# Kernel optimization log

Measured on AMD Instinct MI355X. Metric: run time of the kernel, lower is better.

Reference implementation:

```python
import jax, jax.numpy as jnp
import numpy as np
import math

B, N, E, H = 2, 2048, 1024, 16
K = E // H  # head dim = 64


def setup_inputs() -> dict:
    key = jax.random.key(0)
    ks = jax.random.split(key, 9)
    s = 0.02
    return {
        "x": jax.random.normal(ks[0], (B, N, E), jnp.float32),
        "Wq": jax.random.normal(ks[1], (E, E), jnp.float32) * s,
        "bq": jax.random.normal(ks[2], (E,), jnp.float32) * s,
        "Wk": jax.random.normal(ks[3], (E, E), jnp.float32) * s,
        "bk": jax.random.normal(ks[4], (E,), jnp.float32) * s,
        "Wv": jax.random.normal(ks[5], (E, E), jnp.float32) * s,
        "bv": jax.random.normal(ks[6], (E,), jnp.float32) * s,
        "Wp": jax.random.normal(ks[7], (E, E), jnp.float32) * s,
        "bp": jax.random.normal(ks[8], (E,), jnp.float32) * s,
    }


def _split_heads(t):
    # torch: t.transpose(-1,-2).view(b, H, K, N)  -> (B, H, K, N)
    return t.transpose(0, 2, 1).reshape(t.shape[0], H, K, t.shape[1])


def reference(x, Wq, bq, Wk, bk, Wv, bv, Wp, bp):
    b, n, _ = x.shape
    q = _split_heads(x @ Wq.T + bq)  # (B,H,K,N)
    k = _split_heads(x @ Wk.T + bk)
    v = _split_heads(x @ Wv.T + bv)
    # NOTE: module divides by sqrt(query.size(1)) == sqrt(num_heads), not sqrt(head_dim)
    ctx = jnp.einsum('bhkn,bhkm->bhmn', q, k) / math.sqrt(H)  # (B,H,m=key,n=query)
    mask = jnp.triu(jnp.ones((n, n), dtype=bool), 1)  # True where n(query) > m(key)
    ctx = jnp.where(mask[None, None], -jnp.inf, ctx)
    # faithful to source: softmax over last axis (the query axis n)
    ctx = jax.nn.softmax(ctx, axis=-1)
    out = jnp.einsum('bhmn,bhvm->bhvn', ctx, v)  # (B,H,K,N)
    out = out.reshape(b, E, n).transpose(0, 2, 1)  # (B,N,E)
    return out @ Wp.T + bp
```

## Files before the change

kernel.cpp:

```cpp
#include <hip/hip_runtime.h>
#include <hip/hip_bf16.h>

typedef __hip_bfloat16 bf16;
typedef __attribute__((ext_vector_type(8))) short bf16x8;
typedef __attribute__((ext_vector_type(4))) float f32x4;
typedef __attribute__((ext_vector_type(4))) short s16x4;

constexpr int B_ = 2, N_ = 2048, E_ = 1024, H_ = 16, KD_ = 64;
constexpr int M_ = B_ * N_;
constexpr float SCALE = 0.25f * 1.44269504088896f;

#define MFMA16(A, Bf, C) __builtin_amdgcn_mfma_f32_16x16x32_bf16(A, Bf, C, 0, 0, 0)
#define SBAR() do { __builtin_amdgcn_s_barrier(); __builtin_amdgcn_sched_barrier(0); } while (0)
#define WAITCNT(s) asm volatile("s_waitcnt " s ::: "memory")
#define SETPRIO(p) __builtin_amdgcn_s_setprio(p)

typedef const __attribute__((address_space(1))) void* gptr_t;
typedef __attribute__((address_space(3))) void* sptr_t;

__device__ inline short bf16bits(float f) {
  bf16 h = __float2bfloat16(f);
  short s;
  __builtin_memcpy(&s, &h, 2);
  return s;
}
__device__ inline float bf16f(short s) {
  bf16 h;
  __builtin_memcpy(&h, &s, 2);
  return __bfloat162float(h);
}

template <int NROWS, int NTHR>
__device__ inline void stageT(const bf16* __restrict__ base, int stride_elems,
                              char* lds) {
  const int t = threadIdx.x;
#pragma unroll
  for (int i = 0; i < NROWS * 128 / (NTHR * 16); i++) {
    int L = i * NTHR * 16 + t * 16;
    int row = L >> 7;
    int slot = ((L >> 4) & 7) ^ (row & 7);
    const bf16* src = base + (size_t)row * stride_elems + slot * 8;
    __builtin_amdgcn_global_load_lds((gptr_t)(const void*)src,
                                     (sptr_t)(void*)(lds + L), 16, 0, 0);
  }
}

__device__ inline bf16x8 frag_ld(const char* lds, int row, int ks) {
  const int g = (threadIdx.x >> 4) & 3;
  const int off = (ks * 64 + g * 16) ^ ((row & 7) << 4);
  return *(const bf16x8*)(lds + row * 128 + off);
}

__global__ __launch_bounds__(256) void cvt_all(
    const float* __restrict__ x, const float* __restrict__ wq,
    const float* __restrict__ wk, const float* __restrict__ wv,
    const float* __restrict__ wp, bf16* __restrict__ dst) {
  const size_t XN = (size_t)M_ * E_;
  const size_t WN = (size_t)E_ * E_;
  size_t i = ((size_t)blockIdx.x * 256 + threadIdx.x) * 4;
  const float* src;
  size_t off;
  if (i < XN) { src = x; off = i; }
  else if (i < XN + WN) { src = wq; off = i - XN; }
  else if (i < XN + 2 * WN) { src = wk; off = i - XN - WN; }
  else if (i < XN + 3 * WN) { src = wv; off = i - XN - 2 * WN; }
  else { src = wp; off = i - XN - 3 * WN; }
  float4 v = *(const float4*)(src + off);
  s16x4 o;
  o[0] = bf16bits(v.x); o[1] = bf16bits(v.y);
  o[2] = bf16bits(v.z); o[3] = bf16bits(v.w);
  *(s16x4*)(dst + i) = o;
}

__global__ __launch_bounds__(256) void gemm_qkv(
    const bf16* __restrict__ A, const bf16* __restrict__ Wb,
    const float* __restrict__ bq, const float* __restrict__ bk,
    const float* __restrict__ bv, bf16* __restrict__ Qhd,
    bf16* __restrict__ Khd, bf16* __restrict__ Vtd) {
  __shared__ char Asm[16384];
  __shared__ char Bsm[16384];
  const int t = threadIdx.x, lane = t & 63, w = t >> 6;
  const int wr = w >> 1, wc = w & 1;
  const int c = lane & 15, g = lane >> 4;
  const int row0 = blockIdx.y * 128, col0 = blockIdx.x * 128;
  f32x4 acc[4][4] = {};

  for (int k0 = 0; k0 < E_; k0 += 64) {
    stageT<64, 256>(A + (size_t)row0 * E_ + k0, E_, Asm);
    stageT<64, 256>(A + (size_t)(row0 + 64) * E_ + k0, E_, Asm + 8192);
    stageT<64, 256>(Wb + (size_t)col0 * E_ + k0, E_, Bsm);
    stageT<64, 256>(Wb + (size_t)(col0 + 64) * E_ + k0, E_, Bsm + 8192);
    __syncthreads();
#pragma unroll
    for (int ks = 0; ks < 2; ks++) {
      bf16x8 af[4], bfr[4];
#pragma unroll
      for (int mi = 0; mi < 4; mi++) af[mi] = frag_ld(Asm, wr * 64 + mi * 16 + c, ks);
#pragma unroll
      for (int ni = 0; ni < 4; ni++) bfr[ni] = frag_ld(Bsm, wc * 64 + ni * 16 + c, ks);
#pragma unroll
      for (int mi = 0; mi < 4; mi++)
#pragma unroll
        for (int ni = 0; ni < 4; ni++)
          acc[mi][ni] = MFMA16(af[mi], bfr[ni], acc[mi][ni]);
    }
    __syncthreads();
  }

  const int sel = col0 >> 10;
  const float* biasp = sel == 0 ? bq : sel == 1 ? bk : bv;
  bf16* outp = sel == 0 ? Qhd : sel == 1 ? Khd : Vtd;
#pragma unroll
  for (int mi = 0; mi < 4; mi++) {
#pragma unroll
    for (int ni = 0; ni < 4; ni++) {
      const int row = row0 + wr * 64 + mi * 16 + g * 4;
      const int col = col0 + wc * 64 + ni * 16 + c;
      const int ccol = col & 1023, h = ccol >> 6, kd = ccol & 63;
      const float bvf = biasp[ccol];
      if (sel < 2) {
        const float scl = (sel == 1) ? SCALE : 1.0f;
#pragma unroll
        for (int r = 0; r < 4; r++) {
          const int rr = row + r, b = rr >> 11, n = rr & (N_ - 1);
          outp[(((size_t)(b * H_ + h)) * N_ + n) * KD_ + kd] =
              __float2bfloat16((acc[mi][ni][r] + bvf) * scl);
        }
      } else {
        const int b = row >> 11, n = row & (N_ - 1);
        s16x4 o;
#pragma unroll
        for (int r = 0; r < 4; r++) o[r] = bf16bits(acc[mi][ni][r] + bvf);
        *(s16x4*)&outp[(((size_t)(b * H_ + h)) * KD_ + kd) * N_ + n] = o;
      }
    }
  }
}

__global__ __launch_bounds__(256) void gemm_proj(
    const bf16* __restrict__ A, const bf16* __restrict__ Wb,
    const float* __restrict__ bias, float* __restrict__ outf) {
  __shared__ char Asm[16384];
  __shared__ char Bsm[8192];
  const int t = threadIdx.x, lane = t & 63, w = t >> 6;
  const int wr = w >> 1, wc = w & 1;
  const int c = lane & 15, g = lane >> 4;
  const int row0 = blockIdx.y * 128, col0 = blockIdx.x * 64;
  f32x4 acc[4][2] = {};

  for (int k0 = 0; k0 < E_; k0 += 64) {
    stageT<64, 256>(A + (size_t)row0 * E_ + k0, E_, Asm);
    stageT<64, 256>(A + (size_t)(row0 + 64) * E_ + k0, E_, Asm + 8192);
    stageT<64, 256>(Wb + (size_t)col0 * E_ + k0, E_, Bsm);
    __syncthreads();
#pragma unroll
    for (int ks = 0; ks < 2; ks++) {
      bf16x8 af[4], bfr[2];
#pragma unroll
      for (int mi = 0; mi < 4; mi++) af[mi] = frag_ld(Asm, wr * 64 + mi * 16 + c, ks);
#pragma unroll
      for (int ni = 0; ni < 2; ni++) bfr[ni] = frag_ld(Bsm, wc * 32 + ni * 16 + c, ks);
#pragma unroll
      for (int mi = 0; mi < 4; mi++)
#pragma unroll
        for (int ni = 0; ni < 2; ni++)
          acc[mi][ni] = MFMA16(af[mi], bfr[ni], acc[mi][ni]);
    }
    __syncthreads();
  }

#pragma unroll
  for (int mi = 0; mi < 4; mi++) {
#pragma unroll
    for (int ni = 0; ni < 2; ni++) {
      const int row = row0 + wr * 64 + mi * 16 + g * 4;
      const int col = col0 + wc * 32 + ni * 16 + c;
      const float bvf = bias[col];
#pragma unroll
      for (int r = 0; r < 4; r++)
        outf[(size_t)(row + r) * E_ + col] = acc[mi][ni][r] + bvf;
    }
  }
}

__global__ __launch_bounds__(512, 4) void phaseA(
    const bf16* __restrict__ Kh, const bf16* __restrict__ Qh,
    bf16* __restrict__ Vt) {
  __shared__ char Ksm[8192];
  __shared__ char Qsm[2][16384];
  __shared__ float rbuf[2][64];
  const int t = threadIdx.x, lane = t & 63, w = t >> 6;
  const int c = lane & 15, g = (lane >> 4);
  const int wm = w & 3, wn = w >> 2;
  const int bid = blockIdx.y * 16 + blockIdx.x;
  const int ww = (bid & 7) * 64 + (bid >> 3);
  const int bx = ww & 15, bh = ww >> 4;
  const bf16* Kb = Kh + (size_t)bh * N_ * KD_;
  const bf16* Qb = Qh + (size_t)bh * N_ * KD_;
  bf16* Vtb = Vt + (size_t)bh * KD_ * N_;

#pragma unroll 1
  for (int seg = 0; seg < 2; seg++) {
    const int mb = seg ? (31 - bx) : bx;
    const int m0 = mb * 64;
    const int ntE = mb >> 1;

    WAITCNT("lgkmcnt(0)");
    SBAR();
    stageT<64, 512>(Kb + (size_t)m0 * KD_, KD_, Ksm);
    stageT<128, 512>(Qb, KD_, Qsm[0]);
    WAITCNT("vmcnt(2)");
    SBAR();
    bf16x8 af0 = frag_ld(Ksm, wm * 16 + c, 0);
    bf16x8 af1 = frag_ld(Ksm, wm * 16 + c, 1);
    float sm[4] = {};

#pragma unroll 1
    for (int nt = 0; nt <= ntE; nt++) {
      WAITCNT("vmcnt(0) lgkmcnt(0)");
      SBAR();
      if (nt + 1 <= ntE)
        stageT<128, 512>(Qb + (size_t)(nt + 1) * 128 * KD_, KD_,
                         Qsm[(nt + 1) & 1]);
      const char* qs = Qsm[nt & 1];
      if (nt < ntE) {
#pragma unroll
        for (int nf = 0; nf < 4; nf++) {
          const int ni = wn * 4 + nf;
          bf16x8 b0 = frag_ld(qs, ni * 16 + c, 0);
          bf16x8 b1 = frag_ld(qs, ni * 16 + c, 1);
          SETPRIO(1);
          f32x4 sv = {0.f, 0.f, 0.f, 0.f};
          sv = MFMA16(af0, b0, sv);
          sv = MFMA16(af1, b1, sv);
          SETPRIO(0);
#pragma unroll
          for (int r = 0; r < 4; r++) sm[r] += exp2f(sv[r]);
        }
      } else {
        const int mg = m0 + wm * 16 + g * 4;
#pragma unroll
        for (int nf = 0; nf < 4; nf++) {
          const int ni = wn * 4 + nf;
          bf16x8 b0 = frag_ld(qs, ni * 16 + c, 0);
          bf16x8 b1 = frag_ld(qs, ni * 16 + c, 1);
          SETPRIO(1);
          f32x4 sv = {0.f, 0.f, 0.f, 0.f};
          sv = MFMA16(af0, b0, sv);
          sv = MFMA16(af1, b1, sv);
          SETPRIO(0);
          const int ng = nt * 128 + ni * 16 + c;
#pragma unroll
          for (int r = 0; r < 4; r++) {
            float e = exp2f(sv[r]);
            sm[r] += (ng <= mg + r) ? e : 0.f;
          }
        }
      }
    }

#pragma unroll
    for (int r = 0; r < 4; r++) {
      float v = sm[r];
#pragma unroll
      for (int d = 1; d < 16; d <<= 1) v += __shfl_xor(v, d, 64);
      if (c == 0) rbuf[wn][wm * 16 + g * 4 + r] = v;
    }
    WAITCNT("lgkmcnt(0)");
    SBAR();
    {
      const int kd = t >> 3, mc = (t & 7) * 8;
      bf16* p = Vtb + (size_t)kd * N_ + m0 + mc;
      bf16x8 v = *(const bf16x8*)p;
      bf16x8 o;
#pragma unroll
      for (int j = 0; j < 8; j++) {
        const float inv = 1.0f / (rbuf[0][mc + j] + rbuf[1][mc + j]);
        o[j] = bf16bits(bf16f(v[j]) * inv);
      }
      *(bf16x8*)p = o;
    }
  }
}

__global__ __launch_bounds__(512, 4) void phaseB(
    const bf16* __restrict__ Qh, const bf16* __restrict__ Kh,
    const bf16* __restrict__ Vt, bf16* __restrict__ attn) {
  __shared__ char Ksm[2][8192];
  __shared__ char Vsm[2][8192];
  __shared__ char Psm[8192];
  const int t = threadIdx.x, lane = t & 63, w = t >> 6;
  const int c = lane & 15, g = lane >> 4;
  const int wm = w & 3, wn = w >> 2;
  const int bid = blockIdx.y * 16 + blockIdx.x;
  const int ww = (bid & 7) * 64 + (bid >> 3);
  const int bx = ww & 15, bh = ww >> 4;
  const int b = bh >> 4, h = bh & 15;
  const int NT = N_ / 64;
  const bf16* Qb = Qh + (size_t)bh * N_ * KD_;
  const bf16* Kb = Kh + (size_t)bh * N_ * KD_;
  const bf16* Vb = Vt + (size_t)bh * KD_ * N_;

#pragma unroll 1
  for (int seg = 0; seg < 2; seg++) {
    const int qt = seg ? (31 - bx) : bx;
    const int n0 = qt * 64, mt0 = qt;

    WAITCNT("lgkmcnt(0)");
    SBAR();
    stageT<64, 512>(Qb + (size_t)n0 * KD_, KD_, Psm);
    stageT<64, 512>(Kb + (size_t)mt0 * 64 * KD_, KD_, Ksm[mt0 & 1]);
    stageT<64, 512>(Vb + mt0 * 64, N_, Vsm[mt0 & 1]);
    WAITCNT("vmcnt(2)");
    SBAR();
    bf16x8 qf[2][2];
#pragma unroll
    for (int ni = 0; ni < 2; ni++) {
      qf[ni][0] = frag_ld(Psm, wn * 32 + ni * 16 + c, 0);
      qf[ni][1] = frag_ld(Psm, wn * 32 + ni * 16 + c, 1);
    }
    f32x4 out[2] = {};

    auto do_tile = [&](int mt, bool diag) {
      WAITCNT("vmcnt(0) lgkmcnt(0)");
      SBAR();
      if (mt + 1 < NT) {
        stageT<64, 512>(Kb + (size_t)(mt + 1) * 64 * KD_, KD_, Ksm[(mt + 1) & 1]);
        stageT<64, 512>(Vb + (mt + 1) * 64, N_, Vsm[(mt + 1) & 1]);
      }
      const char* ksm = Ksm[mt & 1];
      bf16x8 kf0 = frag_ld(ksm, wm * 16 + c, 0);
      bf16x8 kf1 = frag_ld(ksm, wm * 16 + c, 1);
      SETPRIO(1);
      f32x4 sv[2];
#pragma unroll
      for (int ni = 0; ni < 2; ni++) {
        f32x4 z = {0.f, 0.f, 0.f, 0.f};
        z = MFMA16(kf0, qf[ni][0], z);
        z = MFMA16(kf1, qf[ni][1], z);
        sv[ni] = z;
      }
      SETPRIO(0);
      const int ml = wm * 16 + g * 4;
#pragma unroll
      for (int ni = 0; ni < 2; ni++) {
        const int nl = wn * 32 + ni * 16 + c;
        s16x4 p;
#pragma unroll
        for (int r = 0; r < 4; r++) {
          float val = exp2f(sv[ni][r]);
          if (diag && nl > (ml + r)) val = 0.f;
          p[r] = bf16bits(val);
        }
        const int off = nl * 128 + ((wm * 32 + g * 8) ^ ((nl & 7) << 4));
        *(s16x4*)(Psm + off) = p;
      }
      WAITCNT("lgkmcnt(0)");
      SBAR();
      const char* vsm = Vsm[mt & 1];
      bf16x8 pa0 = frag_ld(Psm, wm * 16 + c, 0);
      bf16x8 pa1 = frag_ld(Psm, wm * 16 + c, 1);
      SETPRIO(1);
#pragma unroll
      for (int ni = 0; ni < 2; ni++) {
        const int kdrow = wn * 32 + ni * 16 + c;
        bf16x8 v0 = frag_ld(vsm, kdrow, 0);
        bf16x8 v1 = frag_ld(vsm, kdrow, 1);
        out[ni] = MFMA16(pa0, v0, out[ni]);
        out[ni] = MFMA16(pa1, v1, out[ni]);
      }
      SETPRIO(0);
    };

    do_tile(mt0, true);
#pragma unroll 1
    for (int mt = mt0 + 1; mt < NT; mt++) do_tile(mt, false);

#pragma unroll
    for (int ni = 0; ni < 2; ni++) {
#pragma unroll
      for (int r = 0; r < 4; r++) {
        const int n = n0 + wm * 16 + g * 4 + r;
        const int kd = wn * 32 + ni * 16 + c;
        attn[((size_t)(b * N_ + n)) * E_ + h * 64 + kd] =
            __float2bfloat16(out[ni][r]);
      }
    }
  }
}

extern "C" void kernel_launch(void* const* d_in, const int* in_sizes, int n_in,
                              void* d_out, int out_size, void* d_ws, size_t ws_size,
                              hipStream_t stream) {
  (void)in_sizes; (void)n_in; (void)out_size; (void)ws_size;
  const float* x  = (const float*)d_in[0];
  const float* Wq = (const float*)d_in[1];
  const float* bq = (const float*)d_in[2];
  const float* Wk = (const float*)d_in[3];
  const float* bk = (const float*)d_in[4];
  const float* Wv = (const float*)d_in[5];
  const float* bv = (const float*)d_in[6];
  const float* Wp = (const float*)d_in[7];
  const float* bp = (const float*)d_in[8];
  float* out = (float*)d_out;

  const size_t XN = (size_t)M_ * E_;
  const size_t WN = (size_t)E_ * E_;
  const size_t HN = (size_t)B_ * H_ * N_ * KD_;

  bf16* xb   = (bf16*)d_ws;
  bf16* wqkv = xb + XN;
  bf16* wpb  = wqkv + 3 * WN;
  bf16* Qhd  = wpb + WN;
  bf16* Khd  = Qhd + HN;
  bf16* Vtd  = Khd + HN;
  bf16* attn = xb;

  cvt_all<<<dim3(8192), 256, 0, stream>>>(x, Wq, Wk, Wv, Wp, xb);

  gemm_qkv<<<dim3(24, 32), 256, 0, stream>>>(xb, wqkv, bq, bk, bv,
                                             Qhd, Khd, Vtd);

  phaseA<<<dim3(16, B_ * H_), 512, 0, stream>>>(Khd, Qhd, Vtd);
  phaseB<<<dim3(16, B_ * H_), 512, 0, stream>>>(Qhd, Khd, Vtd, attn);

  gemm_proj<<<dim3(16, 32), 256, 0, stream>>>(attn, wpb, bp, out);
}
```

Before: 124.8 us.

## Software-pipeline attention loop: overlap PV of previous tile with QK of current

Splits the per-tile attention body into separate QK and PV stages and interleaves them, so the PV MFMAs for tile mt-1 run alongside the QK and exp work for tile mt. P is double-buffered and V is triple-buffered in shared memory so the prefetched tiles do not overwrite data still being read. This removes one barrier per tile. In exchange, LDS use per block rises from 40 KB to 56 KB, which likely lowers how many blocks fit per CU. The K/V visibility now depends on per-thread vmcnt waits with no barrier before the QK read, which may be a race.

```diff
diff --git a/kernel.cpp b/kernel.cpp
--- a/kernel.cpp
+++ b/kernel.cpp
@@ -287,8 +287,8 @@
     const bf16* __restrict__ Qh, const bf16* __restrict__ Kh,
     const bf16* __restrict__ Vt, bf16* __restrict__ attn) {
   __shared__ char Ksm[2][8192];
-  __shared__ char Vsm[2][8192];
-  __shared__ char Psm[8192];
+  __shared__ char Vsm[3][8192];
+  __shared__ char Psm[2][8192];
   const int t = threadIdx.x, lane = t & 63, w = t >> 6;
   const int c = lane & 15, g = lane >> 4;
   const int wm = w & 3, wn = w >> 2;
@@ -308,26 +308,22 @@
 
     WAITCNT("lgkmcnt(0)");
     SBAR();
-    stageT<64, 512>(Qb + (size_t)n0 * KD_, KD_, Psm);
+    stageT<64, 512>(Qb + (size_t)n0 * KD_, KD_, Psm[0]);
     stageT<64, 512>(Kb + (size_t)mt0 * 64 * KD_, KD_, Ksm[mt0 & 1]);
-    stageT<64, 512>(Vb + mt0 * 64, N_, Vsm[mt0 & 1]);
+    stageT<64, 512>(Vb + mt0 * 64, N_, Vsm[mt0 % 3]);
     WAITCNT("vmcnt(2)");
     SBAR();
     bf16x8 qf[2][2];
 #pragma unroll
     for (int ni = 0; ni < 2; ni++) {
-      qf[ni][0] = frag_ld(Psm, wn * 32 + ni * 16 + c, 0);
-      qf[ni][1] = frag_ld(Psm, wn * 32 + ni * 16 + c, 1);
-    }
+      qf[ni][0] = frag_ld(Psm[0], wn * 32 + ni * 16 + c, 0);
+      qf[ni][1] = frag_ld(Psm[0], wn * 32 + ni * 16 + c, 1);
+    }
+    WAITCNT("lgkmcnt(0)");
+    SBAR();
     f32x4 out[2] = {};
 
-    auto do_tile = [&](int mt, bool diag) {
-      WAITCNT("vmcnt(0) lgkmcnt(0)");
-      SBAR();
-      if (mt + 1 < NT) {
-        stageT<64, 512>(Kb + (size_t)(mt + 1) * 64 * KD_, KD_, Ksm[(mt + 1) & 1]);
-        stageT<64, 512>(Vb + (mt + 1) * 64, N_, Vsm[(mt + 1) & 1]);
-      }
+    auto qk_tile = [&](int mt, bool diag) {
       const char* ksm = Ksm[mt & 1];
       bf16x8 kf0 = frag_ld(ksm, wm * 16 + c, 0);
       bf16x8 kf1 = frag_ld(ksm, wm * 16 + c, 1);
@@ -342,6 +338,7 @@
       }
       SETPRIO(0);
       const int ml = wm * 16 + g * 4;
+      char* ps = Psm[mt & 1];
 #pragma unroll
       for (int ni = 0; ni < 2; ni++) {
         const int nl = wn * 32 + ni * 16 + c;
@@ -353,13 +350,15 @@
           p[r] = bf16bits(val);
         }
         const int off = nl * 128 + ((wm * 32 + g * 8) ^ ((nl & 7) << 4));
-        *(s16x4*)(Psm + off) = p;
-      }
-      WAITCNT("lgkmcnt(0)");
-      SBAR();
-      const char* vsm = Vsm[mt & 1];
-      bf16x8 pa0 = frag_ld(Psm, wm * 16 + c, 0);
-      bf16x8 pa1 = frag_ld(Psm, wm * 16 + c, 1);
+        *(s16x4*)(ps + off) = p;
+      }
+    };
+
+    auto pv_tile = [&](int mt) {
+      const char* ps = Psm[mt & 1];
+      const char* vsm = Vsm[mt % 3];
+      bf16x8 pa0 = frag_ld(ps, wm * 16 + c, 0);
+      bf16x8 pa1 = frag_ld(ps, wm * 16 + c, 1);
       SETPRIO(1);
 #pragma unroll
       for (int ni = 0; ni < 2; ni++) {
@@ -372,9 +371,32 @@
       SETPRIO(0);
     };
 
-    do_tile(mt0, true);
+    if (mt0 + 1 < NT) {
+      stageT<64, 512>(Kb + (size_t)(mt0 + 1) * 64 * KD_, KD_, Ksm[(mt0 + 1) & 1]);
+      stageT<64, 512>(Vb + (mt0 + 1) * 64, N_, Vsm[(mt0 + 1) % 3]);
+      WAITCNT("vmcnt(2)");
+    } else {
+      WAITCNT("vmcnt(0)");
+    }
+    qk_tile(mt0, true);
+
 #pragma unroll 1
-    for (int mt = mt0 + 1; mt < NT; mt++) do_tile(mt, false);
+    for (int mt = mt0 + 1; mt < NT; mt++) {
+      WAITCNT("lgkmcnt(0)");
+      SBAR();
+      if (mt + 1 < NT) {
+        stageT<64, 512>(Kb + (size_t)(mt + 1) * 64 * KD_, KD_, Ksm[(mt + 1) & 1]);
+        stageT<64, 512>(Vb + (mt + 1) * 64, N_, Vsm[(mt + 1) % 3]);
+      }
+      pv_tile(mt - 1);
+      if (mt + 1 < NT) WAITCNT("vmcnt(2)");
+      else WAITCNT("vmcnt(0)");
+      qk_tile(mt, false);
+    }
+
+    WAITCNT("lgkmcnt(0)");
+    SBAR();
+    pv_tile(NT - 1);
 
 #pragma unroll
     for (int ni = 0; ni < 2; ni++) {
```

Measured after the change: 123.0 us, median of 3. About the same (-1.5%).

## Restructure attention phase to 32x32 MFMA, 128-key tiles and in-register P

Applied to the files above, without the earlier changes.

Rewrites the phaseB attention loop to use 32x32x16 MFMA on 128-key tiles, splitting the key dimension across four wave groups. The probabilities stay in registers, rearranged with v_permlane32_swap instead of a round trip through shared memory, which drops a barrier per tile. Partial outputs from the four key groups are then reduced through LDS scratch at the end. LDS use per block grows and the tail adds a multi-step cross-wave reduction, which may lower occupancy.

```diff
diff --git a/kernel.cpp b/kernel.cpp
--- a/kernel.cpp
+++ b/kernel.cpp
@@ -4,19 +4,27 @@
 typedef __hip_bfloat16 bf16;
 typedef __attribute__((ext_vector_type(8))) short bf16x8;
 typedef __attribute__((ext_vector_type(4))) float f32x4;
+typedef __attribute__((ext_vector_type(16))) float f32x16;
 typedef __attribute__((ext_vector_type(4))) short s16x4;
+typedef __attribute__((ext_vector_type(4))) int i32x4;
 
 constexpr int B_ = 2, N_ = 2048, E_ = 1024, H_ = 16, KD_ = 64;
 constexpr int M_ = B_ * N_;
 constexpr float SCALE = 0.25f * 1.44269504088896f;
 
 #define MFMA16(A, Bf, C) __builtin_amdgcn_mfma_f32_16x16x32_bf16(A, Bf, C, 0, 0, 0)
+#define MFMA32(A, Bf, C) __builtin_amdgcn_mfma_f32_32x32x16_bf16(A, Bf, C, 0, 0, 0)
 #define SBAR() do { __builtin_amdgcn_s_barrier(); __builtin_amdgcn_sched_barrier(0); } while (0)
 #define WAITCNT(s) asm volatile("s_waitcnt " s ::: "memory")
 #define SETPRIO(p) __builtin_amdgcn_s_setprio(p)
 
 typedef const __attribute__((address_space(1))) void* gptr_t;
 typedef __attribute__((address_space(3))) void* sptr_t;
+
+__device__ inline void gload16(const bf16* src, char* dst) {
+  __builtin_amdgcn_global_load_lds((gptr_t)(const void*)src,
+                                   (sptr_t)(void*)dst, 16, 0, 0);
+}
 
 __device__ inline short bf16bits(float f) {
   bf16 h = __float2bfloat16(f);
@@ -29,6 +37,14 @@
   __builtin_memcpy(&h, &s, 2);
   return __bfloat162float(h);
 }
+__device__ inline int cvtpk(float a, float b) {
+  int r;
+  asm("v_cvt_pk_bf16_f32 %0, %1, %2" : "=v"(r) : "v"(a), "v"(b));
+  return r;
+}
+__device__ inline void swap32(int& a, int& b) {
+  asm volatile("v_permlane32_swap_b32 %0, %1" : "+v"(a), "+v"(b));
+}
 
 template <int NROWS, int NTHR>
 __device__ inline void stageT(const bf16* __restrict__ base, int stride_elems,
@@ -39,9 +55,7 @@
     int L = i * NTHR * 16 + t * 16;
     int row = L >> 7;
     int slot = ((L >> 4) & 7) ^ (row & 7);
-    const bf16* src = base + (size_t)row * stride_elems + slot * 8;
-    __builtin_amdgcn_global_load_lds((gptr_t)(const void*)src,
-                                     (sptr_t)(void*)(lds + L), 16, 0, 0);
+    gload16(base + (size_t)row * stride_elems + slot * 8, lds + L);
   }
 }
 
@@ -49,6 +63,11 @@
   const int g = (threadIdx.x >> 4) & 3;
   const int off = (ks * 64 + g * 16) ^ ((row & 7) << 4);
   return *(const bf16x8*)(lds + row * 128 + off);
+}
+
+__device__ inline bf16x8 frag_ld256s(const char* lds, int row, int slot) {
+  const int off = (slot * 16) ^ ((row & 15) << 4);
+  return *(const bf16x8*)(lds + row * 256 + off);
 }
 
 __global__ __launch_bounds__(256) void cvt_all(
@@ -286,105 +305,173 @@
 __global__ __launch_bounds__(512, 4) void phaseB(
     const bf16* __restrict__ Qh, const bf16* __restrict__ Kh,
     const bf16* __restrict__ Vt, bf16* __restrict__ attn) {
-  __shared__ char Ksm[2][8192];
-  __shared__ char Vsm[2][8192];
-  __shared__ char Psm[8192];
+  __shared__ char Ksm[2][16384];
+  __shared__ char Vsm[2][16384];
+  __shared__ char Qsm[8192];
   const int t = threadIdx.x, lane = t & 63, w = t >> 6;
-  const int c = lane & 15, g = lane >> 4;
-  const int wm = w & 3, wn = w >> 2;
+  const int c32 = lane & 31, hi = lane >> 5;
+  const int wn = w & 1, mq = w >> 1;
   const int bid = blockIdx.y * 16 + blockIdx.x;
   const int ww = (bid & 7) * 64 + (bid >> 3);
   const int bx = ww & 15, bh = ww >> 4;
   const int b = bh >> 4, h = bh & 15;
-  const int NT = N_ / 64;
+  const int NT = N_ / 128;
   const bf16* Qb = Qh + (size_t)bh * N_ * KD_;
   const bf16* Kb = Kh + (size_t)bh * N_ * KD_;
   const bf16* Vb = Vt + (size_t)bh * KD_ * N_;
 
+  auto stage_kv = [&](int mt) {
+#pragma unroll
+    for (int i = 0; i < 2; i++) {
+      const int L = i * 8192 + t * 16;
+      const int row = L >> 8;
+      const int slot = ((L >> 4) & 15) ^ (row & 15);
+      gload16(Kb + (size_t)(mt * 128 + (slot >> 3) * 64 + row) * KD_ +
+                  (slot & 7) * 8,
+              Ksm[mt & 1] + L);
+    }
+#pragma unroll
+    for (int i = 0; i < 2; i++) {
+      const int L = i * 8192 + t * 16;
+      const int row = L >> 8;
+      const int slot = ((L >> 4) & 15) ^ (row & 15);
+      gload16(Vb + (size_t)row * N_ + mt * 128 + slot * 8, Vsm[mt & 1] + L);
+    }
+  };
+
 #pragma unroll 1
   for (int seg = 0; seg < 2; seg++) {
     const int qt = seg ? (31 - bx) : bx;
-    const int n0 = qt * 64, mt0 = qt;
-
-    WAITCNT("lgkmcnt(0)");
-    SBAR();
-    stageT<64, 512>(Qb + (size_t)n0 * KD_, KD_, Psm);
-    stageT<64, 512>(Kb + (size_t)mt0 * 64 * KD_, KD_, Ksm[mt0 & 1]);
-    stageT<64, 512>(Vb + mt0 * 64, N_, Vsm[mt0 & 1]);
-    WAITCNT("vmcnt(2)");
-    SBAR();
-    bf16x8 qf[2][2];
-#pragma unroll
-    for (int ni = 0; ni < 2; ni++) {
-      qf[ni][0] = frag_ld(Psm, wn * 32 + ni * 16 + c, 0);
-      qf[ni][1] = frag_ld(Psm, wn * 32 + ni * 16 + c, 1);
-    }
-    f32x4 out[2] = {};
-
-    auto do_tile = [&](int mt, bool diag) {
-      WAITCNT("vmcnt(0) lgkmcnt(0)");
-      SBAR();
-      if (mt + 1 < NT) {
-        stageT<64, 512>(Kb + (size_t)(mt + 1) * 64 * KD_, KD_, Ksm[(mt + 1) & 1]);
-        stageT<64, 512>(Vb + (mt + 1) * 64, N_, Vsm[(mt + 1) & 1]);
-      }
+    const int n0 = qt * 64, mt0 = qt >> 1;
+
+    WAITCNT("lgkmcnt(0)");
+    SBAR();
+    {
+      const int L = t * 16, row = L >> 7, slot = ((L >> 4) & 7) ^ (row & 7);
+      gload16(Qb + (size_t)(n0 + row) * KD_ + slot * 8, Qsm + L);
+    }
+    stage_kv(mt0);
+    WAITCNT("vmcnt(4)");
+    SBAR();
+    bf16x8 qf[4];
+    {
+      const int qrow = wn * 32 + c32;
+#pragma unroll
+      for (int s = 0; s < 4; s++) {
+        const int off = ((2 * s + hi) * 16) ^ ((qrow & 7) << 4);
+        qf[s] = *(const bf16x8*)(Qsm + qrow * 128 + off);
+      }
+    }
+    f32x16 acc[2] = {};
+    const int n_gl = n0 + wn * 32 + c32;
+    bf16x8 pfrag[2];
+
+#pragma unroll 1
+    for (int mt = mt0; mt < NT; mt++) {
+      if (mt > mt0) {
+        WAITCNT("lgkmcnt(0)");
+        SBAR();
+      }
+      if (mt + 1 < NT) stage_kv(mt + 1);
+      if (mt + 1 < NT) WAITCNT("vmcnt(4)");
+      else WAITCNT("vmcnt(0)");
+
       const char* ksm = Ksm[mt & 1];
-      bf16x8 kf0 = frag_ld(ksm, wm * 16 + c, 0);
-      bf16x8 kf1 = frag_ld(ksm, wm * 16 + c, 1);
+      const int krow = (mq & 1) * 32 + c32;
+      const int ksb = (mq >> 1) * 8;
       SETPRIO(1);
-      f32x4 sv[2];
-#pragma unroll
-      for (int ni = 0; ni < 2; ni++) {
-        f32x4 z = {0.f, 0.f, 0.f, 0.f};
-        z = MFMA16(kf0, qf[ni][0], z);
-        z = MFMA16(kf1, qf[ni][1], z);
-        sv[ni] = z;
+      f32x16 z = {};
+#pragma unroll
+      for (int s = 0; s < 4; s++) {
+        const int off = ((ksb + 2 * s + hi) * 16) ^ ((krow & 15) << 4);
+        bf16x8 kf = *(const bf16x8*)(ksm + krow * 256 + off);
+        z = MFMA32(kf, qf[s], z);
       }
       SETPRIO(0);
-      const int ml = wm * 16 + g * 4;
-#pragma unroll
-      for (int ni = 0; ni < 2; ni++) {
-        const int nl = wn * 32 + ni * 16 + c;
-        s16x4 p;
-#pragma unroll
-        for (int r = 0; r < 4; r++) {
-          float val = exp2f(sv[ni][r]);
-          if (diag && nl > (ml + r)) val = 0.f;
-          p[r] = bf16bits(val);
+      int wd[4][2];
+      const int mbase = mt * 128 + mq * 32 + 4 * hi;
+      if (mt == mt0) {
+#pragma unroll
+        for (int q = 0; q < 4; q++)
+#pragma unroll
+          for (int p = 0; p < 2; p++) {
+            const int m0g = mbase + 8 * q + 2 * p;
+            float a = (n_gl <= m0g) ? exp2f(z[q * 4 + 2 * p]) : 0.f;
+            float e = (n_gl <= m0g + 1) ? exp2f(z[q * 4 + 2 * p + 1]) : 0.f;
+            wd[q][p] = cvtpk(a, e);
+          }
+      } else {
+#pragma unroll
+        for (int q = 0; q < 4; q++)
+#pragma unroll
+          for (int p = 0; p < 2; p++)
+            wd[q][p] = cvtpk(exp2f(z[q * 4 + 2 * p]), exp2f(z[q * 4 + 2 * p + 1]));
+      }
+#pragma unroll
+      for (int s = 0; s < 2; s++) {
+        int A0 = wd[2 * s][0], B0 = wd[2 * s + 1][0];
+        int A1 = wd[2 * s][1], B1 = wd[2 * s + 1][1];
+        swap32(A0, B0);
+        swap32(A1, B1);
+        i32x4 fr = {A0, A1, B0, B1};
+        __builtin_memcpy(&pfrag[s], &fr, 16);
+      }
+      const char* vsm = Vsm[mt & 1];
+      SETPRIO(1);
+#pragma unroll
+      for (int kb = 0; kb < 2; kb++) {
+        const int vrow = kb * 32 + c32;
+#pragma unroll
+        for (int s = 0; s < 2; s++) {
+          bf16x8 vf = frag_ld256s(vsm, vrow, mq * 4 + 2 * s + hi);
+          acc[kb] = MFMA32(pfrag[s], vf, acc[kb]);
         }
-        const int off = nl * 128 + ((wm * 32 + g * 8) ^ ((nl & 7) << 4));
-        *(s16x4*)(Psm + off) = p;
-      }
-      WAITCNT("lgkmcnt(0)");
-      SBAR();
-      const char* vsm = Vsm[mt & 1];
-      bf16x8 pa0 = frag_ld(Psm, wm * 16 + c, 0);
-      bf16x8 pa1 = frag_ld(Psm, wm * 16 + c, 1);
-      SETPRIO(1);
-#pragma unroll
-      for (int ni = 0; ni < 2; ni++) {
-        const int kdrow = wn * 32 + ni * 16 + c;
-        bf16x8 v0 = frag_ld(vsm, kdrow, 0);
-        bf16x8 v1 = frag_ld(vsm, kdrow, 1);
-        out[ni] = MFMA16(pa0, v0, out[ni]);
-        out[ni] = MFMA16(pa1, v1, out[ni]);
       }
       SETPRIO(0);
-    };
-
-    do_tile(mt0, true);
-#pragma unroll 1
-    for (int mt = mt0 + 1; mt < NT; mt++) do_tile(mt, false);
-
-#pragma unroll
-    for (int ni = 0; ni < 2; ni++) {
-#pragma unroll
-      for (int r = 0; r < 4; r++) {
-        const int n = n0 + wm * 16 + g * 4 + r;
-        const int kd = wn * 32 + ni * 16 + c;
-        attn[((size_t)(b * N_ + n)) * E_ + h * 64 + kd] =
-            __float2bfloat16(out[ni][r]);
-      }
+    }
+
+    float* scr = (float*)&Ksm[0][0];
+    float* scr2 = (float*)&Vsm[0][0];
+    WAITCNT("lgkmcnt(0)");
+    SBAR();
+    if (mq >= 2) {
+      float* rg = scr + ((mq - 2) * 2 + wn) * 2048;
+#pragma unroll
+      for (int kb = 0; kb < 2; kb++)
+#pragma unroll
+        for (int i = 0; i < 16; i++) rg[(kb * 16 + i) * 64 + lane] = acc[kb][i];
+    }
+    WAITCNT("lgkmcnt(0)");
+    SBAR();
+    if (mq < 2) {
+      float* rg = scr + (mq * 2 + wn) * 2048;
+#pragma unroll
+      for (int kb = 0; kb < 2; kb++)
+#pragma unroll
+        for (int i = 0; i < 16; i++) acc[kb][i] += rg[(kb * 16 + i) * 64 + lane];
+    }
+    WAITCNT("lgkmcnt(0)");
+    SBAR();
+    if (mq == 1) {
+      float* rg = scr2 + wn * 2048;
+#pragma unroll
+      for (int kb = 0; kb < 2; kb++)
+#pragma unroll
+        for (int i = 0; i < 16; i++) rg[(kb * 16 + i) * 64 + lane] = acc[kb][i];
+    }
+    WAITCNT("lgkmcnt(0)");
+    SBAR();
+    if (mq == 0) {
+      float* rg = scr2 + wn * 2048;
+#pragma unroll
+      for (int kb = 0; kb < 2; kb++)
+#pragma unroll
+        for (int i = 0; i < 16; i++) {
+          const float v = acc[kb][i] + rg[(kb * 16 + i) * 64 + lane];
+          const int n = n0 + wn * 32 + (i & 3) + 8 * (i >> 2) + 4 * hi;
+          const int kd = kb * 32 + c32;
+          attn[((size_t)(b * N_ + n)) * E_ + h * 64 + kd] = __float2bfloat16(v);
+        }
     }
   }
 }
```

After: 124.5 us. Within noise of the previous version (-0.2%).
